# Optimization experiments

Measured on AMD Instinct MI355X. Metric: run time of the kernel, lower is better.

Reference implementation:

```python
import jax, jax.numpy as jnp
import numpy as np

# Marching-tetrahedra lookup tables (from DMTet.__init__)
TRIANGLE_TABLE = jnp.array([
    [-1,-1,-1,-1,-1,-1],[1,0,2,-1,-1,-1],[4,0,3,-1,-1,-1],[1,4,2,1,3,4],
    [3,1,5,-1,-1,-1],[2,3,0,2,5,3],[1,4,0,1,5,4],[4,2,5,-1,-1,-1],
    [4,5,2,-1,-1,-1],[4,1,0,4,5,1],[3,2,0,3,5,2],[1,3,5,-1,-1,-1],
    [4,1,2,4,3,1],[3,0,4,-1,-1,-1],[2,0,1,-1,-1,-1],[-1,-1,-1,-1,-1,-1]], dtype=jnp.int32)
NUM_TRIANGLES_TABLE = jnp.array([0,1,1,2,1,2,2,1,1,2,2,1,2,1,1,0], dtype=jnp.int32)
BASE_TET_EDGES = jnp.array([0,1,0,2,0,3,1,2,1,3,2,3], dtype=jnp.int32)
NUM_TETS_TABLE = jnp.array([0,1,1,3,1,3,3,3,1,3,3,3,3,3,3,1], dtype=jnp.int32)
TET_TABLE = jnp.array([
    [-1,-1,-1,-1,-1,-1,-1,-1,-1,-1,-1,-1],
    [0,4,5,6,-1,-1,-1,-1,-1,-1,-1,-1],
    [1,4,8,7,-1,-1,-1,-1,-1,-1,-1,-1],
    [7,1,8,6,5,1,7,6,5,0,1,6],
    [2,5,7,9,-1,-1,-1,-1,-1,-1,-1,-1],
    [4,0,6,7,9,0,7,6,7,0,9,2],
    [4,1,9,8,5,1,9,4,5,1,2,9],
    [6,0,1,2,8,6,1,2,9,6,8,2],
    [3,6,9,8,-1,-1,-1,-1,-1,-1,-1,-1],
    [5,0,4,8,5,0,8,3,5,8,9,3],
    [1,4,7,3,4,7,6,3,9,6,7,3],
    [0,1,5,3,5,1,9,3,5,1,7,9],
    [5,2,3,7,3,6,5,8,3,5,7,8],
    [0,4,7,8,0,3,8,7,0,3,7,2],
    [4,1,2,3,4,3,2,5,4,3,5,6],
    [0,1,2,3,-1,-1,-1,-1,-1,-1,-1,-1]], dtype=jnp.int32)


def _structure(sdf, indices):
    """All integer / topology computation (torch.no_grad region).
    Returns interp_v [E,2] crossing edges, uniq vertex ids, remapped tets.
    Runs eagerly (data-dependent shapes, matching torch.unique semantics)."""
    N = sdf.shape[0]
    occ = sdf > 0                                   # [N]
    occ_fx4 = occ[indices]                          # [F,4]
    occ_sum = occ_fx4.sum(-1)
    valid = (occ_sum > 0) & (occ_sum < 4)
    valid_tets = indices[valid]                     # [Fv,4]
    occ_valid = occ_fx4[valid]
    # per-tet edges, sorted so (min,max) -> matches DMTet.sort_edges
    e = valid_tets[:, BASE_TET_EDGES].reshape(-1, 2)
    e = jnp.stack([jnp.minimum(e[:, 0], e[:, 1]), jnp.maximum(e[:, 0], e[:, 1])], -1)
    ue, idx_map = jnp.unique(e, axis=0, return_inverse=True)   # lexicographic, like torch.unique(dim=0)
    idx_map = idx_map.reshape(-1)
    mask_edges = occ[ue].sum(-1) == 1               # sign-crossing edges
    mapping = jnp.where(mask_edges, jnp.cumsum(mask_edges) - 1, -1)
    idx_map = mapping[idx_map].reshape(-1, 6)       # [Fv,6] new-vertex ids (or -1)
    interp_v = ue[mask_edges]                       # [E,2]
    tetindex = (occ_valid.astype(jnp.int32) * jnp.array([1, 2, 4, 8], dtype=jnp.int32)).sum(-1)
    num_tets = NUM_TETS_TABLE[tetindex]
    tve = jnp.concatenate([valid_tets, idx_map + N], axis=1)   # [Fv,10]
    mt1 = num_tets == 1
    mt3 = num_tets == 3
    side_tets = jnp.concatenate([
        jnp.take_along_axis(tve[mt1], TET_TABLE[tetindex[mt1], :4].astype(tve.dtype), axis=1).reshape(-1, 4),
        jnp.take_along_axis(tve[mt3], TET_TABLE[tetindex[mt3], :12].astype(tve.dtype), axis=1).reshape(-1, 4)], axis=0)
    inner_tets = indices[occ_sum == 4]
    all_tets = jnp.concatenate([side_tets, inner_tets], axis=0)
    uniq, inv = jnp.unique(all_tets.reshape(-1), return_inverse=True)
    return interp_v, uniq, inv.reshape(-1, 4)


def setup_inputs() -> dict:
    N, F = 300000, 1500000
    key = jax.random.key(0)
    k1, k2, k3, k4 = jax.random.split(key, 4)
    verts = jax.random.normal(k1, (N, 3), dtype=jnp.float32)
    deform = jax.random.normal(k2, (N, 3), dtype=jnp.float32)
    sdf = jax.random.normal(k3, (N,), dtype=jnp.float32)
    indices = jax.random.randint(k4, (F, 4), 0, N)
    return {"verts": verts, "deform": deform, "sdf": sdf, "indices": indices, "grid_res": 128}


def reference(verts, deform, sdf, indices, grid_res):
    interp_v, uniq, tets = _structure(sdf, indices)
    # v_deformed = verts + 2/(2*res) * tanh(deform)
    pos = verts + (2.0 / (grid_res * 2)) * jnp.tanh(deform)
    # edge interpolation: v = p1*(-s2) / (s1 - s2) + p2*s1 / (s1 - s2)
    e_pos = pos[interp_v]                            # [E,2,3]
    e_sdf = sdf[interp_v] * jnp.array([1.0, -1.0], dtype=sdf.dtype)  # [s1, -s2]
    w = e_sdf[:, ::-1] / e_sdf.sum(-1, keepdims=True)               # flip / denom
    new_verts = (e_pos * w[..., None]).sum(1)        # [E,3]
    all_verts = jnp.concatenate([pos, new_verts], axis=0)
    return all_verts[uniq], tets
```

## Files before the change

kernel.cpp:

```cpp
#include <hip/hip_runtime.h>
#include <stdint.h>

typedef unsigned int u32;
typedef unsigned long long u64;
typedef unsigned short u16;
typedef unsigned char u8;

#define CTR_M 0
#define CTR_E 1
#define CTR_C1 2
#define CTR_C3 3
#define CTR_CI 4
#define CTR_T 5
#define CTR_U 6
#define CTR_OUT1 7

#define RWIN 4096
#define RROUNDS (RWIN / 1024)

__device__ const u64 TETPACK[16] = {
  0xFFFFFFFFFFFFULL,
  0xFFFFFFFF6540ULL,
  0xFFFFFFFF7841ULL,
  0x610567156817ULL,
  0xFFFFFFFF9752ULL,
  0x290767097604ULL,
  0x921549158914ULL,
  0x286921682106ULL,
  0xFFFFFFFF8963ULL,
  0x398538058405ULL,
  0x376936743741ULL,
  0x971539153510ULL,
  0x875385637325ULL,
  0x273078308740ULL,
  0x653452343214ULL,
  0xFFFFFFFF3210ULL
};

__device__ __forceinline__ u32 bscan256(u32 x, u32* s4, u32& total)
{
  const int lane = threadIdx.x & 63;
  const int wid = threadIdx.x >> 6;
  u32 incl = x;
  #pragma unroll
  for (int d = 1; d < 64; d <<= 1) {
    u32 t = __shfl_up(incl, d);
    if (lane >= d) incl += t;
  }
  if (lane == 63) s4[wid] = incl;
  __syncthreads();
  u32 w0 = s4[0], w1 = s4[1], w2 = s4[2], w3 = s4[3];
  total = w0 + w1 + w2 + w3;
  u32 off = (wid > 0 ? w0 : 0u) + (wid > 1 ? w1 : 0u) + (wid > 2 ? w2 : 0u);
  return off + incl;
}

__device__ __forceinline__ u64 bscan256_64(u64 x, u64* s4, u64& total)
{
  const int lane = threadIdx.x & 63;
  const int wid = threadIdx.x >> 6;
  u64 incl = x;
  #pragma unroll
  for (int d = 1; d < 64; d <<= 1) {
    u64 t = __shfl_up(incl, d);
    if (lane >= d) incl += t;
  }
  if (lane == 63) s4[wid] = incl;
  __syncthreads();
  u64 w0 = s4[0], w1 = s4[1], w2 = s4[2], w3 = s4[3];
  total = w0 + w1 + w2 + w3;
  u64 off = (wid > 0 ? w0 : 0ull) + (wid > 1 ? w1 : 0ull) + (wid > 2 ? w2 : 0ull);
  return off + incl;
}

__global__ void __launch_bounds__(256) k_pos(
    const float* __restrict__ verts, const float* __restrict__ deform,
    const float* __restrict__ sdf, const int* __restrict__ grptr,
    float* __restrict__ pos, u32* __restrict__ occw, int N, int n3)
{
  int i = blockIdx.x * 256 + threadIdx.x;
  if (i < n3) {
    float inv = 1.0f / (float)grptr[0];
    pos[i] = verts[i] + tanhf(deform[i]) * inv;
  }
  const int NOCC = (N + 1023) / 1024;
  if (blockIdx.x < NOCC) {
    __shared__ u32 s_nib[256];
    const int tid = threadIdx.x;
    int base = blockIdx.x * 1024 + tid * 4;
    u32 nib = 0;
    if (base + 3 < N) {
      float4 s = *reinterpret_cast<const float4*>(sdf + base);
      nib = (s.x > 0.0f ? 1u : 0u) | (s.y > 0.0f ? 2u : 0u) |
            (s.z > 0.0f ? 4u : 0u) | (s.w > 0.0f ? 8u : 0u);
    } else {
      for (int k = 0; k < 4; ++k)
        if (base + k < N) nib |= (sdf[base + k] > 0.0f ? 1u : 0u) << k;
    }
    s_nib[tid] = nib;
    __syncthreads();
    if (tid < 32) {
      u32 w = 0;
      #pragma unroll
      for (int j = 0; j < 8; ++j) w |= s_nib[tid * 8 + j] << (4 * j);
      int wi = blockIdx.x * 32 + tid;
      if (wi < (N + 31) / 32) occw[wi] = w;
    }
  }
}

__global__ void __launch_bounds__(256) k_classify(
    const int* __restrict__ idx, const u32* __restrict__ occw, int F,
    u64* __restrict__ A, u32* __restrict__ ctr,
    u64* __restrict__ bsF, u8* __restrict__ tetidx, u8* __restrict__ flag)
{
  const int tid = threadIdx.x;
  const int lane = tid & 63;
  const int wid = tid >> 6;
  const int base = blockIdx.x * 1024 + tid * 4;
  u32 tis4 = 0;
  u32 cms[4];
  int4 vs[4];
  u64 cnt = 0;
  u32 ec = 0;
  #pragma unroll
  for (int it = 0; it < 4; ++it) {
    const int f = base + it;
    u32 ti = 0, cm = 0;
    int4 v = make_int4(0, 0, 0, 0);
    if (f < F) {
      v = reinterpret_cast<const int4*>(idx)[f];
      u32 b0 = (occw[(u32)v.x >> 5] >> (v.x & 31)) & 1u;
      u32 b1 = (occw[(u32)v.y >> 5] >> (v.y & 31)) & 1u;
      u32 b2 = (occw[(u32)v.z >> 5] >> (v.z & 31)) & 1u;
      u32 b3 = (occw[(u32)v.w >> 5] >> (v.w & 31)) & 1u;
      if (b0) flag[v.x] = 1;
      if (b1) flag[v.y] = 1;
      if (b2) flag[v.z] = 1;
      if (b3) flag[v.w] = 1;
      ti = b0 | (b1 << 1) | (b2 << 2) | (b3 << 3);
      cm  = (b0 ^ b1);
      cm |= (b0 ^ b2) << 1;
      cm |= (b0 ^ b3) << 2;
      cm |= (b1 ^ b2) << 3;
      cm |= (b1 ^ b3) << 4;
      cm |= (b2 ^ b3) << 5;
      int pc = __popc(ti);
      if (pc == 1) cnt += 1ULL;
      else if (pc == 2 || pc == 3) cnt += (1ULL << 21);
      else if (pc == 4) cnt += (1ULL << 42);
    }
    vs[it] = v;
    cms[it] = cm;
    tis4 |= ti << (8 * it);
    ec += __popc(cm);
  }
  u32 incl = ec;
  #pragma unroll
  for (int d = 1; d < 64; d <<= 1) {
    u32 t = __shfl_up(incl, d);
    if (lane >= d) incl += t;
  }
  u32 excl = incl - ec;
  __shared__ u32 s_wtot[4];
  __shared__ u32 s_base;
  if (lane == 63) s_wtot[wid] = incl;
  __syncthreads();
  if (tid == 0) {
    u32 t0 = s_wtot[0], t1 = s_wtot[1], t2 = s_wtot[2], t3 = s_wtot[3];
    u32 tot = t0 + t1 + t2 + t3;
    s_base = tot ? atomicAdd(&ctr[CTR_M], tot) : 0u;
    s_wtot[0] = 0; s_wtot[1] = t0; s_wtot[2] = t0 + t1; s_wtot[3] = t0 + t1 + t2;
  }
  __syncthreads();
  u32 w = s_base + s_wtot[wid] + excl;
  #pragma unroll
  for (int it = 0; it < 4; ++it) {
    u32 cm = cms[it];
    if (!cm) continue;
    const int f = base + it;
    const int va[6] = {vs[it].x, vs[it].x, vs[it].x, vs[it].y, vs[it].y, vs[it].z};
    const int vb[6] = {vs[it].y, vs[it].z, vs[it].w, vs[it].z, vs[it].w, vs[it].w};
    #pragma unroll
    for (int s = 0; s < 6; ++s) {
      if ((cm >> s) & 1u) {
        int a = va[s], b = vb[s];
        int mn = min(a, b), mx = max(a, b);
        u64 key = ((u64)(u32)mn << 19) | (u64)(u32)mx;
        A[w++] = (key << 24) | (u64)(u32)(f * 6 + s);
      }
    }
  }
  if (base < F) {
    if (base + 3 < F) {
      *reinterpret_cast<u32*>(tetidx + base) = tis4;
    } else {
      for (int it = 0; it < 4; ++it)
        if (base + it < F) tetidx[base + it] = (u8)((tis4 >> (8 * it)) & 255u);
    }
  }
  u64 r = cnt;
  #pragma unroll
  for (int d = 32; d > 0; d >>= 1) r += __shfl_xor(r, d);
  __shared__ u64 s_w64[4];
  if (lane == 0) s_w64[wid] = r;
  __syncthreads();
  if (tid == 0) bsF[blockIdx.x] = s_w64[0] + s_w64[1] + s_w64[2] + s_w64[3];
}

__global__ void __launch_bounds__(256) k_hist4(
    const u64* __restrict__ A, const u32* __restrict__ ctr, u32* __restrict__ gh)
{
  __shared__ u32 sh[1344];
  const int tid = threadIdx.x;
  for (int b = tid; b < 1344; b += 256) sh[b] = 0;
  __syncthreads();
  const int M = (int)ctr[CTR_M];
  for (int i = blockIdx.x * 256 + tid; i < M; i += gridDim.x * 256) {
    u64 v = A[i];
    atomicAdd(&sh[        (u32)(v >> 24) & 255u], 1u);
    atomicAdd(&sh[ 256 + ((u32)(v >> 32) & 255u)], 1u);
    atomicAdd(&sh[ 512 + ((u32)(v >> 40) & 255u)], 1u);
    atomicAdd(&sh[ 768 + ((u32)(v >> 48) & 255u)], 1u);
    atomicAdd(&sh[1024 + ((u32)(v >> 56) &  63u)], 1u);
    atomicAdd(&sh[1088 + ((u32)(v >> 16) & 255u)], 1u);
  }
  __syncthreads();
  for (int b = tid; b < 1344; b += 256) if (sh[b]) atomicAdd(&gh[b], sh[b]);
}

__global__ void __launch_bounds__(256) k_scan4(u32* __restrict__ gh)
{
  __shared__ u32 s4[4];
  const int tid = threadIdx.x;
  const int off[6] = {0, 256, 512, 768, 1024, 1088};
  const int len[6] = {256, 256, 256, 256, 64, 256};
  for (int s = 0; s < 6; ++s) {
    u32 v = (tid < len[s]) ? gh[off[s] + tid] : 0u;
    u32 total;
    u32 incl = bscan256(v, s4, total);
    if (tid < len[s]) gh[off[s] + tid] = incl - v;
    __syncthreads();
  }
}

__global__ void __launch_bounds__(256) k_rowscan(
    u32* __restrict__ hist, int NBR, const u32* __restrict__ gh)
{
  const int d = blockIdx.x;
  u32* row = hist + (size_t)d * NBR;
  const int tid = threadIdx.x;
  __shared__ u32 s4[4];
  u32 carry = gh[d];
  for (int start = 0; start < NBR; start += 256) {
    int i = start + tid;
    u32 v = (i < NBR) ? row[i] : 0u;
    u32 total;
    u32 incl = bscan256(v, s4, total);
    if (i < NBR) row[i] = carry + incl - v;
    carry += total;
    __syncthreads();
  }
}

__global__ void __launch_bounds__(1024) k_scanF(
    u64* __restrict__ bsF, int nb, u32* __restrict__ ctr)
{
  __shared__ u64 sh16[16];
  const int tid = threadIdx.x;
  const int lane = tid & 63;
  const int wid = tid >> 6;
  u64 carry = 0;
  for (int start = 0; start < nb; start += 1024) {
    int i = start + tid;
    u64 v = (i < nb) ? bsF[i] : 0ULL;
    u64 incl = v;
    #pragma unroll
    for (int d = 1; d < 64; d <<= 1) {
      u64 t = __shfl_up(incl, d);
      if (lane >= d) incl += t;
    }
    if (lane == 63) sh16[wid] = incl;
    __syncthreads();
    if (wid == 0) {
      u64 w = (lane < 16) ? sh16[lane] : 0ull;
      #pragma unroll
      for (int d = 1; d < 16; d <<= 1) {
        u64 t = __shfl_up(w, d);
        if (lane >= d) w += t;
      }
      if (lane < 16) sh16[lane] = w;
    }
    __syncthreads();
    u64 waveoff = (wid > 0) ? sh16[wid - 1] : 0ull;
    u64 total = sh16[15];
    if (i < nb) bsF[i] = carry + waveoff + incl - v;
    carry += total;
    __syncthreads();
  }
  if (tid == 0) {
    u32 c1 = (u32)(carry & 0x1FFFFFULL);
    u32 c3 = (u32)((carry >> 21) & 0x1FFFFFULL);
    u32 ci = (u32)((carry >> 42) & 0x1FFFFFULL);
    ctr[CTR_C1] = c1; ctr[CTR_C3] = c3; ctr[CTR_CI] = ci;
    ctr[CTR_T] = c1 + 3u * c3 + ci;
  }
}

__global__ void __launch_bounds__(256) k_rowbase(
    const u8* __restrict__ tetidx, const u64* __restrict__ bsF,
    const u32* __restrict__ ctr, int F, int* __restrict__ rowbase)
{
  const int tid = threadIdx.x;
  const int base = blockIdx.x * 1024 + tid * 4;
  u32 tis[4];
  u64 cnt = 0;
  #pragma unroll
  for (int it = 0; it < 4; ++it) {
    int f = base + it;
    u32 ti = (f < F) ? (u32)tetidx[f] : 0u;
    tis[it] = ti;
    int pc = __popc(ti);
    if (ti) {
      if (pc == 1) cnt += 1ULL;
      else if (pc <= 3) cnt += (1ULL << 21);
      else cnt += (1ULL << 42);
    }
  }
  __shared__ u64 s4[4];
  u64 total;
  u64 incl = bscan256_64(cnt, s4, total);
  u64 off = bsF[blockIdx.x] + (incl - cnt);
  u32 o1 = (u32)(off & 0x1FFFFFULL);
  u32 o3 = (u32)((off >> 21) & 0x1FFFFFULL);
  u32 oi = (u32)((off >> 42) & 0x1FFFFFULL);
  const u32 C1 = ctr[CTR_C1], C3 = ctr[CTR_C3];
  int rb[4];
  #pragma unroll
  for (int it = 0; it < 4; ++it) {
    u32 ti = tis[it];
    int pc = __popc(ti);
    int r = -1;
    if (ti == 15u) { r = (int)(C1 + 3u * C3 + oi); ++oi; }
    else if (ti) {
      if (pc == 1) { r = (int)o1; ++o1; }
      else { r = (int)(C1 + 3u * o3); ++o3; }
    }
    rb[it] = r;
  }
  if (base + 3 < F) {
    reinterpret_cast<int4*>(rowbase)[base >> 2] = make_int4(rb[0], rb[1], rb[2], rb[3]);
  } else {
    for (int it = 0; it < 4; ++it)
      if (base + it < F) rowbase[base + it] = rb[it];
  }
}

__global__ void __launch_bounds__(256) k_hist(
    const u64* __restrict__ src, const u32* __restrict__ ctr,
    int shift, int nbits, u32* __restrict__ hist, int NBR)
{
  const int NB = 1 << nbits;
  __shared__ u32 sh[256];
  const int tid = threadIdx.x;
  if (tid < NB) sh[tid] = 0;
  __syncthreads();
  const int M = (int)ctr[CTR_M];
  const int base = blockIdx.x * RWIN;
  for (int r = 0; r < RROUNDS; ++r) {
    int rbase = base + r * 1024;
    if (rbase >= M) break;
    int ib = rbase + tid * 4;
    #pragma unroll
    for (int j = 0; j < 4; ++j) {
      if (ib + j < M) {
        u32 d = (u32)(src[ib + j] >> shift) & (u32)(NB - 1);
        atomicAdd(&sh[d], 1u);
      }
    }
  }
  __syncthreads();
  if (tid < NB) hist[tid * NBR + blockIdx.x] = sh[tid];
}

__device__ __forceinline__ u32 block_scan_incl_1024(u32 x, u32* shtmp, u32& total)
{
  const int lane = threadIdx.x & 63;
  const int wid = threadIdx.x >> 6;
  u32 incl = x;
  #pragma unroll
  for (int d = 1; d < 64; d <<= 1) {
    u32 t = __shfl_up(incl, d);
    if (lane >= d) incl += t;
  }
  if (lane == 63) shtmp[wid] = incl;
  __syncthreads();
  if (wid == 0) {
    u32 w = (lane < 16) ? shtmp[lane] : 0u;
    #pragma unroll
    for (int d = 1; d < 16; d <<= 1) {
      u32 t = __shfl_up(w, d);
      if (lane >= d) w += t;
    }
    if (lane < 16) shtmp[lane] = w;
  }
  __syncthreads();
  u32 waveoff = (wid > 0) ? shtmp[wid - 1] : 0u;
  total = shtmp[15];
  return waveoff + incl;
}

__global__ void __launch_bounds__(1024) k_scan_u32(
    u32* __restrict__ data, int L, u32* __restrict__ ctr, int slot)
{
  __shared__ u32 shtmp[16];
  const int tid = threadIdx.x;
  u32 carry = 0;
  for (int start = 0; start < L; start += 4096) {
    u32 v[4]; u32 s = 0;
    #pragma unroll
    for (int j = 0; j < 4; ++j) {
      int i = start + tid * 4 + j;
      v[j] = (i < L) ? data[i] : 0u;
      s += v[j];
    }
    u32 total;
    u32 incl = block_scan_incl_1024(s, shtmp, total);
    u32 run = carry + incl - s;
    #pragma unroll
    for (int j = 0; j < 4; ++j) {
      int i = start + tid * 4 + j;
      if (i < L) data[i] = run;
      run += v[j];
    }
    carry += total;
    __syncthreads();
  }
  if (slot >= 0 && tid == 0) ctr[slot] = carry;
}

__device__ __forceinline__ void scatter_body(
    const u64* __restrict__ src, u64* __restrict__ dst,
    const u32* __restrict__ ctr, int shift, int NBITS,
    const u32* __restrict__ hist, int NBR,
    u32* s_gbase, u16* s_wh)
{
  const int NB = 1 << NBITS;
  const int tid = threadIdx.x;
  const int lane = tid & 63;
  const int wid = tid >> 6;
  if (tid < NB) s_gbase[tid] = hist[tid * NBR + blockIdx.x];
  for (int b = tid; b < NB * 8; b += 256) reinterpret_cast<u32*>(s_wh)[b] = 0;
  __syncthreads();
  const int M = (int)ctr[CTR_M];
  const u64 lowmask = (1ULL << lane) - 1ULL;
  const int base = blockIdx.x * RWIN;
  for (int r = 0; r < RROUNDS; ++r) {
    int rbase = base + r * 1024;
    if (rbase >= M) break;
    u64 v[4]; u32 d4[4]; u32 lr4[4]; bool act[4];
    #pragma unroll
    for (int j = 0; j < 4; ++j) {
      int ib = rbase + (wid * 4 + j) * 64 + lane;
      act[j] = ib < M;
      v[j] = act[j] ? src[ib] : 0ULL;
      d4[j] = (u32)(v[j] >> shift) & (u32)(NB - 1);
    }
    #pragma unroll
    for (int j = 0; j < 4; ++j) {
      u32 d = d4[j];
      u64 mask = __ballot(act[j]);
      for (int b = 0; b < NBITS; ++b) {
        u64 bal = __ballot(act[j] && ((d >> b) & 1u));
        mask &= ((d >> b) & 1u) ? bal : ~bal;
      }
      lr4[j] = (u32)__popcll(mask & lowmask);
      if (act[j] && lr4[j] == 0)
        s_wh[(wid * 4 + j) * NB + d] = (u16)__popcll(mask);
    }
    __syncthreads();
    u32 mytot = 0;
    if (tid < NB) {
      u32 run = 0;
      #pragma unroll
      for (int s = 0; s < 16; ++s) {
        u32 c = (u32)s_wh[s * NB + tid];
        s_wh[s * NB + tid] = (u16)run;
        run += c;
      }
      mytot = run;
    }
    __syncthreads();
    #pragma unroll
    for (int j = 0; j < 4; ++j) {
      if (!act[j]) continue;
      u32 d = d4[j];
      dst[s_gbase[d] + (u32)s_wh[(wid * 4 + j) * NB + d] + lr4[j]] = v[j];
    }
    __syncthreads();
    if (tid < NB) {
      s_gbase[tid] += mytot;
      #pragma unroll
      for (int s = 0; s < 16; ++s) s_wh[s * NB + tid] = 0;
    }
    __syncthreads();
  }
}

__global__ void __launch_bounds__(256) k_scatter8(
    const u64* __restrict__ src, u64* __restrict__ dst,
    const u32* __restrict__ ctr, int shift,
    const u32* __restrict__ hist, int NBR)
{
  __shared__ u32 s_gbase[256];
  __shared__ u16 s_wh[16 * 256];
  scatter_body(src, dst, ctr, shift, 8, hist, NBR, s_gbase, s_wh);
}

__global__ void __launch_bounds__(256) k_scatter6(
    const u64* __restrict__ src, u64* __restrict__ dst,
    const u32* __restrict__ ctr, int shift,
    const u32* __restrict__ hist, int NBR)
{
  __shared__ u32 s_gbase[64];
  __shared__ u16 s_wh[16 * 64];
  scatter_body(src, dst, ctr, shift, 6, hist, NBR, s_gbase, s_wh);
}

__global__ void __launch_bounds__(256) k_headcount(
    const u64* __restrict__ S, const u32* __restrict__ ctr, u32* __restrict__ bsE)
{
  const int tid = threadIdx.x;
  const int lane = tid & 63;
  const int wid = tid >> 6;
  const int M = (int)ctr[CTR_M];
  if (blockIdx.x * 1024 >= M) {
    if (tid == 0) bsE[blockIdx.x] = 0;
    return;
  }
  const int base = blockIdx.x * 1024 + tid * 4;
  u32 c = 0;
  u64 prev = (base > 0 && base < M) ? (S[base - 1] >> 24) : 0ULL;
  #pragma unroll
  for (int j = 0; j < 4; ++j) {
    int i = base + j;
    if (i < M) {
      u64 k = S[i] >> 24;
      c += ((i == 0) || (k != prev)) ? 1u : 0u;
      prev = k;
    }
  }
  #pragma unroll
  for (int d = 32; d > 0; d >>= 1) c += __shfl_xor(c, d);
  __shared__ u32 s4[4];
  if (lane == 0) s4[wid] = c;
  __syncthreads();
  if (tid == 0) bsE[blockIdx.x] = s4[0] + s4[1] + s4[2] + s4[3];
}

__global__ void __launch_bounds__(256) k_assign(
    const u64* __restrict__ S, const u32* __restrict__ ctr,
    const u32* __restrict__ bsE, u64* __restrict__ stage,
    u32* __restrict__ hist, int NBR, u64* __restrict__ edgekeys)
{
  const int tid = threadIdx.x;
  const int M = (int)ctr[CTR_M];
  if (blockIdx.x * 1024 >= M) return;
  const int base = blockIdx.x * 1024 + tid * 4;
  __shared__ u32 s_h[256];
  __shared__ u32 s4[4];
  s_h[tid] = 0;
  u64 v[4]; bool hd[4];
  u32 c = 0;
  u64 prev = (base > 0 && base < M) ? (S[base - 1] >> 24) : 0ULL;
  #pragma unroll
  for (int j = 0; j < 4; ++j) {
    int i = base + j;
    v[j] = (i < M) ? S[i] : 0ULL;
    u64 k = v[j] >> 24;
    hd[j] = (i < M) && ((i == 0) || (k != prev));
    if (i < M) prev = k;
    c += hd[j] ? 1u : 0u;
  }
  u32 total;
  u32 incl = bscan256(c, s4, total);
  u32 run = bsE[blockIdx.x] + incl - c;
  #pragma unroll
  for (int j = 0; j < 4; ++j) {
    int i = base + j;
    if (i < M) {
      run += hd[j] ? 1u : 0u;
      u32 id = run - 1u;
      if (hd[j]) edgekeys[id] = v[j] >> 24;
      u32 pay = (u32)(v[j] & 0xFFFFFFULL);
      stage[i] = ((u64)pay << 24) | (u64)id;
      atomicAdd(&s_h[(pay >> 16) & 255u], 1u);
    }
  }
  __syncthreads();
  if (s_h[tid]) atomicAdd(&hist[tid * NBR + (blockIdx.x >> 2)], s_h[tid]);
}

__global__ void __launch_bounds__(256) k_deliver(
    const u64* __restrict__ D, const u32* __restrict__ ctr,
    int* __restrict__ edge_ids)
{
  int i = blockIdx.x * 256 + threadIdx.x;
  if (i >= (int)ctr[CTR_M]) return;
  u64 c = D[i];
  edge_ids[(u32)(c >> 24)] = (int)(c & 0xFFFFFFULL);
}

__global__ void __launch_bounds__(1024) k_scanbits(
    const u32* __restrict__ flag32, u64* __restrict__ bwr,
    int W, u32* __restrict__ ctr)
{
  __shared__ u32 shtmp[16];
  const int tid = threadIdx.x;
  u32 carry = 0;
  for (int start = 0; start < W; start += 1024) {
    int w = start + tid;
    u32 bits = 0;
    if (w < W) {
      #pragma unroll
      for (int k = 0; k < 8; ++k) {
        u32 fo = flag32[w * 8 + k];
        u32 nib = (fo & 1u) | ((fo >> 7) & 2u) | ((fo >> 14) & 4u) | ((fo >> 21) & 8u);
        bits |= nib << (4 * k);
      }
    }
    u32 c = (u32)__popc(bits);
    u32 total;
    u32 incl = block_scan_incl_1024(c, shtmp, total);
    if (w < W) bwr[w] = (u64)bits | ((u64)(carry + incl - c) << 32);
    carry += total;
    __syncthreads();
  }
  if (tid == 0) {
    ctr[CTR_U] = carry;
    ctr[CTR_OUT1] = 3u * (carry + ctr[CTR_E]);
  }
}

__global__ void __launch_bounds__(256) k_out0_orig(
    const u64* __restrict__ bwr, const float* __restrict__ pos,
    int N, float* __restrict__ out)
{
  int id = blockIdx.x * 256 + threadIdx.x;
  if (id >= N) return;
  u64 bw = bwr[(u32)id >> 5];
  u32 bits = (u32)bw;
  if (!((bits >> (id & 31)) & 1u)) return;
  u32 j = (u32)(bw >> 32) + (u32)__popc(bits & ((1u << (id & 31)) - 1u));
  size_t o = (size_t)3 * j;
  out[o] = pos[3 * id]; out[o + 1] = pos[3 * id + 1]; out[o + 2] = pos[3 * id + 2];
}

__global__ void __launch_bounds__(256) k_out0_edge(
    const u64* __restrict__ edgekeys, const float* __restrict__ pos,
    const float* __restrict__ sdf, const u32* __restrict__ ctr,
    float* __restrict__ out)
{
  int e = blockIdx.x * 256 + threadIdx.x;
  if (e >= (int)ctr[CTR_E]) return;
  u64 k = edgekeys[e];
  int a = (int)(k >> 19);
  int b = (int)(k & 0x7FFFFULL);
  float sa = sdf[a], sb = sdf[b];
  float inv = 1.0f / (sa - sb);
  float wa = -sb * inv, wb = sa * inv;
  u32 j = ctr[CTR_U] + (u32)e;
  size_t o = (size_t)3 * j;
  out[o]     = pos[3 * a] * wa + pos[3 * b] * wb;
  out[o + 1] = pos[3 * a + 1] * wa + pos[3 * b + 1] * wb;
  out[o + 2] = pos[3 * a + 2] * wa + pos[3 * b + 2] * wb;
}

__global__ void __launch_bounds__(256) k_out1(
    const int* __restrict__ idx, const u8* __restrict__ tetidx,
    const int* __restrict__ edge_ids, const int* __restrict__ rowbase,
    const u64* __restrict__ bwr, const u32* __restrict__ ctr,
    int F, int N, float* __restrict__ out)
{
  int f = blockIdx.x * 256 + threadIdx.x;
  if (f >= F) return;
  u32 ti = tetidx[f];
  if (ti == 0) return;
  int4 v = reinterpret_cast<const int4*>(idx)[f];
  int pc = __popc(ti);
  int nt = (pc == 1 || pc == 4) ? 1 : 3;
  u64 row = TETPACK[ti];
  u32 obase = ctr[CTR_OUT1];
  u32 U0 = ctr[CTR_U];
  int rb = rowbase[f];
  float cr[4] = {0.f, 0.f, 0.f, 0.f};
  const int ids[4] = {v.x, v.y, v.z, v.w};
  #pragma unroll
  for (int c = 0; c < 4; ++c) {
    if ((ti >> c) & 1u) {
      int id = ids[c];
      u64 bw = bwr[(u32)id >> 5];
      cr[c] = (float)((u32)(bw >> 32) + (u32)__popc((u32)bw & ((1u << (id & 31)) - 1u)));
    }
  }
  const bool al16 = (obase & 3u) == 0u;
  float* outp = out + (size_t)obase + (size_t)rb * 4;
  for (int t = 0; t < nt; ++t) {
    u32 quad = (u32)(row >> (16 * t)) & 0xFFFFu;
    float o[4];
    #pragma unroll
    for (int k = 0; k < 4; ++k) {
      u32 e = (quad >> (4 * k)) & 15u;
      o[k] = (e < 4u) ? cr[e] : (float)(U0 + (u32)edge_ids[f * 6 + (int)(e - 4u)]);
    }
    if (al16) {
      *reinterpret_cast<float4*>(outp + (size_t)t * 4) =
          make_float4(o[0], o[1], o[2], o[3]);
    } else {
      __builtin_memcpy(outp + (size_t)t * 4, o, 16);
    }
  }
}

extern "C" void kernel_launch(void* const* d_in, const int* in_sizes, int n_in,
                              void* d_out, int out_size, void* d_ws, size_t ws_size,
                              hipStream_t stream)
{
  const float* verts  = (const float*)d_in[0];
  const float* deform = (const float*)d_in[1];
  const float* sdf    = (const float*)d_in[2];
  const int* indices  = (const int*)d_in[3];
  const int* grptr    = (const int*)d_in[4];
  const int N = in_sizes[2];
  const int F = in_sizes[3] / 4;
  const int MMAX = 4 * F;
  const int NBF = (F + 1023) / 1024;
  const int NBR = (MMAX + RWIN - 1) / RWIN;
  const int NBA = (MMAX + 1023) / 1024;
  const int W = (N + 31) / 32;

  char* p = (char*)d_ws;
  auto take = [&](size_t bytes) {
    char* r = p;
    p += (bytes + 255) & ~(size_t)255;
    return r;
  };
  u32* ctr       = (u32*)take(256);
  u32* gh        = (u32*)take(1344 * 4);
  u64* A         = (u64*)take((size_t)MMAX * 8);
  u64* B         = (u64*)take((size_t)MMAX * 8);
  u64* EK        = (u64*)take((size_t)MMAX * 8);
  int* edge_ids  = (int*)take((size_t)F * 6 * 4);
  float* pos     = (float*)take((size_t)N * 3 * 4);
  int* rowbase   = (int*)take((size_t)F * 4);
  u8* tetidx     = (u8*)take((size_t)F);
  u32* hist      = (u32*)take((size_t)NBR * 256 * 4);
  u32* bsE       = (u32*)take((size_t)NBA * 4);
  u64* bsF       = (u64*)take((size_t)NBF * 8);
  u8* flag       = (u8*)take((size_t)W * 32);
  u32* occw      = (u32*)take((size_t)W * 4);
  u64* bwr       = (u64*)take((size_t)W * 8);
  if ((size_t)(p - (char*)d_ws) > ws_size) return;

  hipMemsetAsync(ctr, 0, 256, stream);
  hipMemsetAsync(gh, 0, 1344 * 4, stream);
  hipMemsetAsync(flag, 0, (size_t)W * 32, stream);

  float* out = (float*)d_out;

  k_pos<<<(N * 3 + 255) / 256, 256, 0, stream>>>(verts, deform, sdf, grptr,
                                                 pos, occw, N, N * 3);
  k_classify<<<NBF, 256, 0, stream>>>(indices, occw, F, A, ctr, bsF, tetidx, flag);
  k_scanF<<<1, 1024, 0, stream>>>(bsF, NBF, ctr);
  k_rowbase<<<NBF, 256, 0, stream>>>(tetidx, bsF, ctr, F, rowbase);

  k_hist4<<<2048, 256, 0, stream>>>(A, ctr, gh);
  k_scan4<<<1, 256, 0, stream>>>(gh);

  const int shifts[5] = {24, 32, 40, 48, 56};
  const int nbitsv[5] = {8, 8, 8, 8, 6};
  const int ghoff[5]  = {0, 256, 512, 768, 1024};
  u64* src = A; u64* dst = B;
  for (int pass = 0; pass < 5; ++pass) {
    k_hist<<<NBR, 256, 0, stream>>>(src, ctr, shifts[pass], nbitsv[pass], hist, NBR);
    k_rowscan<<<(1 << nbitsv[pass]), 256, 0, stream>>>(hist, NBR, gh + ghoff[pass]);
    if (nbitsv[pass] == 8)
      k_scatter8<<<NBR, 256, 0, stream>>>(src, dst, ctr, shifts[pass], hist, NBR);
    else
      k_scatter6<<<NBR, 256, 0, stream>>>(src, dst, ctr, shifts[pass], hist, NBR);
    u64* t = src; src = dst; dst = t;
  }
  const u64* S = src;
  u64* stage = dst;

  k_headcount<<<NBA, 256, 0, stream>>>(S, ctr, bsE);
  k_scan_u32<<<1, 1024, 0, stream>>>(bsE, NBA, ctr, CTR_E);
  hipMemsetAsync(hist, 0, (size_t)NBR * 256 * 4, stream);
  k_assign<<<NBA, 256, 0, stream>>>(S, ctr, bsE, stage, hist, NBR, EK);
  k_rowscan<<<256, 256, 0, stream>>>(hist, NBR, gh + 1088);
  k_scatter8<<<NBR, 256, 0, stream>>>(stage, (u64*)S, ctr, 40, hist, NBR);
  k_deliver<<<(MMAX + 255) / 256, 256, 0, stream>>>(S, ctr, edge_ids);

  k_scanbits<<<1, 1024, 0, stream>>>((const u32*)flag, bwr, W, ctr);
  k_out0_orig<<<(N + 255) / 256, 256, 0, stream>>>(bwr, pos, N, out);
  k_out0_edge<<<(MMAX + 255) / 256, 256, 0, stream>>>(EK, pos, sdf, ctr, out);
  k_out1<<<(F + 255) / 256, 256, 0, stream>>>(indices, tetidx, edge_ids, rowbase,
                                              bwr, ctr, F, N, out);
}
```

Before: 609.1 us.

## Stage radix scatter through LDS and pad key arrays to remove bounds checks

The radix-sort scatter now writes each 1024-key round into a shared-memory buffer ordered by digit, then writes to global memory from that buffer so stores to each bucket are contiguous. Key arrays are padded with all-ones sentinels up to the window size so the histogram and scatter kernels can skip per-element bounds checks and ballot masking. The padding keys sort to the end and fall outside M, so later kernels should ignore them. The cost is an extra LDS pass, a block scan and more barriers per round, plus a small extra padding kernel.

```diff
diff --git a/kernel.cpp b/kernel.cpp
--- a/kernel.cpp
+++ b/kernel.cpp
@@ -208,6 +208,15 @@
   if (tid == 0) bsF[blockIdx.x] = s_w64[0] + s_w64[1] + s_w64[2] + s_w64[3];
 }
 
+__global__ void __launch_bounds__(256) k_pad(
+    u64* __restrict__ A, const u32* __restrict__ ctr)
+{
+  const u32 M = ctr[CTR_M];
+  const u32 Mp = (M + RWIN - 1) & ~(u32)(RWIN - 1);
+  u32 i = M + blockIdx.x * 256 + threadIdx.x;
+  if (i < Mp) A[i] = ~0ULL;
+}
+
 __global__ void __launch_bounds__(256) k_hist4(
     const u64* __restrict__ A, const u32* __restrict__ ctr, u32* __restrict__ gh)
 {
@@ -361,22 +370,21 @@
     int shift, int nbits, u32* __restrict__ hist, int NBR)
 {
   const int NB = 1 << nbits;
+  const u32 M = ctr[CTR_M];
+  const u32 Mp = (M + RWIN - 1) & ~(u32)(RWIN - 1);
+  const u32 base = blockIdx.x * RWIN;
+  if (base >= Mp) return;
   __shared__ u32 sh[256];
   const int tid = threadIdx.x;
   if (tid < NB) sh[tid] = 0;
   __syncthreads();
-  const int M = (int)ctr[CTR_M];
-  const int base = blockIdx.x * RWIN;
+  #pragma unroll
   for (int r = 0; r < RROUNDS; ++r) {
-    int rbase = base + r * 1024;
-    if (rbase >= M) break;
-    int ib = rbase + tid * 4;
+    u32 ib = base + r * 1024 + tid * 4;
     #pragma unroll
     for (int j = 0; j < 4; ++j) {
-      if (ib + j < M) {
-        u32 d = (u32)(src[ib + j] >> shift) & (u32)(NB - 1);
-        atomicAdd(&sh[d], 1u);
-      }
+      u32 d = (u32)(src[ib + j] >> shift) & (u32)(NB - 1);
+      atomicAdd(&sh[d], 1u);
     }
   }
   __syncthreads();
@@ -439,39 +447,42 @@
   if (slot >= 0 && tid == 0) ctr[slot] = carry;
 }
 
+template<int NBITS, bool PADDED>
 __device__ __forceinline__ void scatter_body(
     const u64* __restrict__ src, u64* __restrict__ dst,
-    const u32* __restrict__ ctr, int shift, int NBITS,
+    const u32* __restrict__ ctr, int shift,
     const u32* __restrict__ hist, int NBR,
-    u32* s_gbase, u16* s_wh)
+    u32* s_gbase, u16* s_wh, u64* s_stage, u32* s_drs, u32* s4)
 {
   const int NB = 1 << NBITS;
   const int tid = threadIdx.x;
   const int lane = tid & 63;
   const int wid = tid >> 6;
+  const u32 M = ctr[CTR_M];
+  const u32 Mp = PADDED ? ((M + RWIN - 1) & ~(u32)(RWIN - 1)) : M;
+  const u32 base = blockIdx.x * RWIN;
+  if (base >= Mp) return;
   if (tid < NB) s_gbase[tid] = hist[tid * NBR + blockIdx.x];
   for (int b = tid; b < NB * 8; b += 256) reinterpret_cast<u32*>(s_wh)[b] = 0;
   __syncthreads();
-  const int M = (int)ctr[CTR_M];
   const u64 lowmask = (1ULL << lane) - 1ULL;
-  const int base = blockIdx.x * RWIN;
   for (int r = 0; r < RROUNDS; ++r) {
-    int rbase = base + r * 1024;
-    if (rbase >= M) break;
+    u32 rbase = base + r * 1024;
+    if (rbase >= Mp) break;
     u64 v[4]; u32 d4[4]; u32 lr4[4]; bool act[4];
     #pragma unroll
     for (int j = 0; j < 4; ++j) {
-      int ib = rbase + (wid * 4 + j) * 64 + lane;
-      act[j] = ib < M;
-      v[j] = act[j] ? src[ib] : 0ULL;
+      u32 ib = rbase + (wid * 4 + j) * 64 + lane;
+      act[j] = PADDED ? true : (ib < M);
+      v[j] = act[j] ? src[ib] : ~0ULL;
       d4[j] = (u32)(v[j] >> shift) & (u32)(NB - 1);
     }
     #pragma unroll
     for (int j = 0; j < 4; ++j) {
       u32 d = d4[j];
-      u64 mask = __ballot(act[j]);
+      u64 mask = PADDED ? ~0ULL : __ballot(act[j]);
       for (int b = 0; b < NBITS; ++b) {
-        u64 bal = __ballot(act[j] && ((d >> b) & 1u));
+        u64 bal = __ballot(((d >> b) & 1u) != 0u);
         mask &= ((d >> b) & 1u) ? bal : ~bal;
       }
       lr4[j] = (u32)__popcll(mask & lowmask);
@@ -490,12 +501,26 @@
       }
       mytot = run;
     }
+    u32 dtot;
+    u32 dincl = bscan256(mytot, s4, dtot);
+    if (tid < NB) s_drs[tid] = dincl - mytot;
     __syncthreads();
     #pragma unroll
     for (int j = 0; j < 4; ++j) {
       if (!act[j]) continue;
       u32 d = d4[j];
-      dst[s_gbase[d] + (u32)s_wh[(wid * 4 + j) * NB + d] + lr4[j]] = v[j];
+      u32 lpos = s_drs[d] + (u32)s_wh[(wid * 4 + j) * NB + d] + lr4[j];
+      s_stage[lpos] = v[j];
+    }
+    __syncthreads();
+    #pragma unroll
+    for (int k = 0; k < 4; ++k) {
+      u32 i = k * 256u + (u32)tid;
+      if (i < dtot) {
+        u64 vv = s_stage[i];
+        u32 d = (u32)(vv >> shift) & (u32)(NB - 1);
+        dst[s_gbase[d] + (i - s_drs[d])] = vv;
+      }
     }
     __syncthreads();
     if (tid < NB) {
@@ -507,24 +532,46 @@
   }
 }
 
-__global__ void __launch_bounds__(256) k_scatter8(
+__global__ void __launch_bounds__(256) k_scatter8p(
     const u64* __restrict__ src, u64* __restrict__ dst,
     const u32* __restrict__ ctr, int shift,
     const u32* __restrict__ hist, int NBR)
 {
   __shared__ u32 s_gbase[256];
   __shared__ u16 s_wh[16 * 256];
-  scatter_body(src, dst, ctr, shift, 8, hist, NBR, s_gbase, s_wh);
-}
-
-__global__ void __launch_bounds__(256) k_scatter6(
+  __shared__ u64 s_stage[1024];
+  __shared__ u32 s_drs[256];
+  __shared__ u32 s4[4];
+  scatter_body<8, true>(src, dst, ctr, shift, hist, NBR,
+                        s_gbase, s_wh, s_stage, s_drs, s4);
+}
+
+__global__ void __launch_bounds__(256) k_scatter8m(
     const u64* __restrict__ src, u64* __restrict__ dst,
     const u32* __restrict__ ctr, int shift,
     const u32* __restrict__ hist, int NBR)
 {
+  __shared__ u32 s_gbase[256];
+  __shared__ u16 s_wh[16 * 256];
+  __shared__ u64 s_stage[1024];
+  __shared__ u32 s_drs[256];
+  __shared__ u32 s4[4];
+  scatter_body<8, false>(src, dst, ctr, shift, hist, NBR,
+                         s_gbase, s_wh, s_stage, s_drs, s4);
+}
+
+__global__ void __launch_bounds__(256) k_scatter6p(
+    const u64* __restrict__ src, u64* __restrict__ dst,
+    const u32* __restrict__ ctr, int shift,
+    const u32* __restrict__ hist, int NBR)
+{
   __shared__ u32 s_gbase[64];
   __shared__ u16 s_wh[16 * 64];
-  scatter_body(src, dst, ctr, shift, 6, hist, NBR, s_gbase, s_wh);
+  __shared__ u64 s_stage[1024];
+  __shared__ u32 s_drs[64];
+  __shared__ u32 s4[4];
+  scatter_body<6, true>(src, dst, ctr, shift, hist, NBR,
+                        s_gbase, s_wh, s_stage, s_drs, s4);
 }
 
 __global__ void __launch_bounds__(256) k_headcount(
@@ -747,8 +794,8 @@
   };
   u32* ctr       = (u32*)take(256);
   u32* gh        = (u32*)take(1344 * 4);
-  u64* A         = (u64*)take((size_t)MMAX * 8);
-  u64* B         = (u64*)take((size_t)MMAX * 8);
+  u64* A         = (u64*)take((size_t)NBR * RWIN * 8);
+  u64* B         = (u64*)take((size_t)NBR * RWIN * 8);
   u64* EK        = (u64*)take((size_t)MMAX * 8);
   int* edge_ids  = (int*)take((size_t)F * 6 * 4);
   float* pos     = (float*)take((size_t)N * 3 * 4);
@@ -771,6 +818,7 @@
   k_pos<<<(N * 3 + 255) / 256, 256, 0, stream>>>(verts, deform, sdf, grptr,
                                                  pos, occw, N, N * 3);
   k_classify<<<NBF, 256, 0, stream>>>(indices, occw, F, A, ctr, bsF, tetidx, flag);
+  k_pad<<<RWIN / 256, 256, 0, stream>>>(A, ctr);
   k_scanF<<<1, 1024, 0, stream>>>(bsF, NBF, ctr);
   k_rowbase<<<NBF, 256, 0, stream>>>(tetidx, bsF, ctr, F, rowbase);
 
@@ -785,9 +833,9 @@
     k_hist<<<NBR, 256, 0, stream>>>(src, ctr, shifts[pass], nbitsv[pass], hist, NBR);
     k_rowscan<<<(1 << nbitsv[pass]), 256, 0, stream>>>(hist, NBR, gh + ghoff[pass]);
     if (nbitsv[pass] == 8)
-      k_scatter8<<<NBR, 256, 0, stream>>>(src, dst, ctr, shifts[pass], hist, NBR);
+      k_scatter8p<<<NBR, 256, 0, stream>>>(src, dst, ctr, shifts[pass], hist, NBR);
     else
-      k_scatter6<<<NBR, 256, 0, stream>>>(src, dst, ctr, shifts[pass], hist, NBR);
+      k_scatter6p<<<NBR, 256, 0, stream>>>(src, dst, ctr, shifts[pass], hist, NBR);
     u64* t = src; src = dst; dst = t;
   }
   const u64* S = src;
@@ -798,7 +846,7 @@
   hipMemsetAsync(hist, 0, (size_t)NBR * 256 * 4, stream);
   k_assign<<<NBA, 256, 0, stream>>>(S, ctr, bsE, stage, hist, NBR, EK);
   k_rowscan<<<256, 256, 0, stream>>>(hist, NBR, gh + 1088);
-  k_scatter8<<<NBR, 256, 0, stream>>>(stage, (u64*)S, ctr, 40, hist, NBR);
+  k_scatter8m<<<NBR, 256, 0, stream>>>(stage, (u64*)S, ctr, 40, hist, NBR);
   k_deliver<<<(MMAX + 255) / 256, 256, 0, stream>>>(S, ctr, edge_ids);
 
   k_scanbits<<<1, 1024, 0, stream>>>((const u32*)flag, bwr, W, ctr);
```

After: 598.4 us (median of 3 runs). No clear change (-1.8%).
